# Optimization experiments

Hardware: AMD Instinct MI355X
Metric: run time of the kernel (lower is better)

The kernel has to match this reference:

```python
import jax, jax.numpy as jnp
import numpy as np

N_NODES = 100000
N_EDGES = 3200000
IN_FEATS = 512
HIDDEN = 256
N_CLASSES = 64
NITER = 10
HALT_BIAS_INIT = 3.0


def setup_inputs() -> dict:
    key = jax.random.key(0)
    ks = jax.random.split(key, 8)
    x = jax.random.normal(ks[0], (N_NODES, IN_FEATS), dtype=jnp.float32)
    edge_index = jax.random.randint(ks[1], (2, N_EDGES), 0, N_NODES, dtype=jnp.int64)
    # Linear layers: layers[0]: in->hidden, layers[1]: hidden->classes, halt: classes->1
    W0 = jax.random.normal(ks[2], (IN_FEATS, HIDDEN), dtype=jnp.float32) / np.sqrt(IN_FEATS)
    b0 = jnp.zeros((HIDDEN,), dtype=jnp.float32)
    W1 = jax.random.normal(ks[3], (HIDDEN, N_CLASSES), dtype=jnp.float32) / np.sqrt(HIDDEN)
    b1 = jnp.zeros((N_CLASSES,), dtype=jnp.float32)
    Wh = jax.random.normal(ks[4], (N_CLASSES, 1), dtype=jnp.float32) / np.sqrt(N_CLASSES)
    bh = jnp.full((1,), HALT_BIAS_INIT, dtype=jnp.float32)
    return {"x": x, "edge_index": edge_index, "edge_dropout": 0,
            "W0": W0, "b0": b0, "W1": W1, "b1": b1, "Wh": Wh, "bh": bh}


def reference(x, edge_index, edge_dropout, W0, b0, W1, b1, Wh, bh):
    N = x.shape[0]
    # MLP encoder (eval mode: dropout is identity)
    h = jax.nn.relu(x @ W0 + b0)
    h = h @ W1 + b1                                   # [N, C]

    # gcn_norm with self-loops (edge_dropout=0 in eval => identical every iter)
    loops = jnp.arange(N, dtype=edge_index.dtype)
    row = jnp.concatenate([edge_index[0], loops])     # source
    col = jnp.concatenate([edge_index[1], loops])     # target (aggregation index)
    deg = jax.ops.segment_sum(jnp.ones_like(col, dtype=h.dtype), col, num_segments=N)
    dinv = jnp.where(deg > 0, deg ** -0.5, 0.0)
    norm = dinv[row] * dinv[col]                      # [E+N]

    def step(ph, _):
        msg = norm[:, None] * ph[row]                 # gather + scale, [E+N, C]
        ph2 = jax.ops.segment_sum(msg, col, num_segments=N)  # scatter_add
        logit = jnp.clip(ph2 @ Wh + bh, -10.0, 10.0)  # [N, 1]
        return ph2, (ph2, logit)

    _, (props, logits) = jax.lax.scan(step, h, None, length=NITER)
    outputs = jnp.concatenate([h[None], props], axis=0)       # [niter+1, N, C]
    halting_logits = jnp.transpose(logits[:, :, 0])           # [N, niter]

    lam = jax.nn.sigmoid(halting_logits)
    remain = jnp.cumprod(1.0 - lam, axis=1)                   # inclusive
    remain_excl = jnp.concatenate([jnp.ones((N, 1), lam.dtype), remain[:, :-1]], axis=1)
    p = lam * remain_excl
    p = p.at[:, -1].add(remain[:, -1])                        # leftover mass to last step
    return outputs, p, halting_logits
```

## Files before the change

### kernel.cpp

```cpp
#include <hip/hip_runtime.h>
#include <hip/hip_bf16.h>

#define N_NODES  100000
#define N_EDGES  3200000
#define IN_FEATS 512
#define HIDDEN   256
#define N_CLASSES 64
#define NITER    10

#define SCAN_NB  49

#define OUT_P_OFF  ((size_t)(NITER + 1) * N_NODES * N_CLASSES)
#define OUT_HL_OFF (OUT_P_OFF + (size_t)N_NODES * NITER)

#define WS_META_INTS (4 * N_NODES + 128)
#define WS_CSR_OFF   ((size_t)WS_META_INTS * 4)
#define WS_W0F_OFF   (WS_CSR_OFF + (size_t)2 * N_EDGES * 4)
#define WS_W1F_OFF   (WS_W0F_OFF + 262144)
#define WS_SH0_OFF   (WS_W1F_OFF + 32768)
#define WS_SH1_OFF   (WS_SH0_OFF + (size_t)N_NODES * 64 * 2)
#define WS_NEED_W    (WS_SH0_OFF)
#define WS_NEED_BF   (WS_SH1_OFF + (size_t)N_NODES * 64 * 2)

typedef _Float16 f16x8 __attribute__((ext_vector_type(8)));
typedef _Float16 f16x4 __attribute__((ext_vector_type(4)));
typedef float    f32x4 __attribute__((ext_vector_type(4)));

__device__ __forceinline__ float bflo(unsigned v) { return __uint_as_float(v << 16); }
__device__ __forceinline__ float bfhi(unsigned v) { return __uint_as_float(v & 0xffff0000u); }
__device__ __forceinline__ unsigned short f2bf(float f) {
    unsigned u = __float_as_uint(f);
    return (unsigned short)((u + 0x7fffu + ((u >> 16) & 1u)) >> 16);
}

__global__ void k_detect(const int* ei, int* flag) {
    if (threadIdx.x == 0 && blockIdx.x == 0) {
        int is64 = 1;
        for (int k = 0; k < 128; ++k) {
            if (ei[2 * k + 1] != 0) { is64 = 0; break; }
        }
        *flag = is64;
    }
}

__device__ __forceinline__ int edge_row(const void* ei, int is64, int e) {
    return is64 ? (int)((const long long*)ei)[e] : ((const int*)ei)[e];
}
__device__ __forceinline__ int edge_col(const void* ei, int is64, int e) {
    return is64 ? (int)((const long long*)ei)[(size_t)N_EDGES + e]
                : ((const int*)ei)[(size_t)N_EDGES + e];
}
__device__ __forceinline__ int edge_row_nt(const void* ei, int is64, int e) {
    return is64 ? (int)__builtin_nontemporal_load((const long long*)ei + e)
                : __builtin_nontemporal_load((const int*)ei + e);
}
__device__ __forceinline__ int edge_col_nt(const void* ei, int is64, int e) {
    return is64 ? (int)__builtin_nontemporal_load((const long long*)ei + (size_t)N_EDGES + e)
                : __builtin_nontemporal_load((const int*)ei + (size_t)N_EDGES + e);
}

__global__ void k_count(const void* ei, const int* flag, int* cnt) {
    int e = blockIdx.x * 256 + threadIdx.x;
    if (e >= N_EDGES) return;
    int is64 = *flag;
    atomicAdd(&cnt[edge_col_nt(ei, is64, e)], 1);
}

__global__ __launch_bounds__(256) void k_scan1(const int* cnt, int* part) {
    __shared__ int sd[256];
    int b = blockIdx.x, t = threadIdx.x;
    int s = 0;
    for (int j = t; j < 2048; j += 256) {
        int idx = b * 2048 + j;
        if (idx < N_NODES) s += cnt[idx];
    }
    sd[t] = s;
    __syncthreads();
    for (int o = 128; o > 0; o >>= 1) {
        if (t < o) sd[t] += sd[t + o];
        __syncthreads();
    }
    if (t == 0) part[b] = sd[0];
}

__global__ __launch_bounds__(256) void k_scan2(int* part, int* offs) {
    __shared__ int sd[256];
    int t = threadIdx.x;
    sd[t] = (t < SCAN_NB) ? part[t] : 0;
    __syncthreads();
    for (int o = 1; o < 256; o <<= 1) {
        int add = (t >= o) ? sd[t - o] : 0;
        __syncthreads();
        sd[t] += add;
        __syncthreads();
    }
    if (t < SCAN_NB) part[t] = (t == 0) ? 0 : sd[t - 1];
    if (t == 0) offs[N_NODES] = N_EDGES;
}

__global__ __launch_bounds__(256) void k_scan3(const int* cnt, const int* part, int* offs) {
    __shared__ int sd[256];
    int b = blockIdx.x, t = threadIdx.x;
    int base = b * 2048 + t * 8;
    int local[8];
    int s = 0;
#pragma unroll
    for (int j = 0; j < 8; ++j) {
        int idx = base + j;
        int v = (idx < N_NODES) ? cnt[idx] : 0;
        local[j] = s;
        s += v;
    }
    sd[t] = s;
    __syncthreads();
    for (int o = 1; o < 256; o <<= 1) {
        int add = (t >= o) ? sd[t - o] : 0;
        __syncthreads();
        sd[t] += add;
        __syncthreads();
    }
    int tbase = part[b] + ((t == 0) ? 0 : sd[t - 1]);
#pragma unroll
    for (int j = 0; j < 8; ++j) {
        int idx = base + j;
        if (idx < N_NODES) offs[idx] = tbase + local[j];
    }
}

__global__ void k_dinv(const int* cnt, float* dinv) {
    int i = blockIdx.x * 256 + threadIdx.x;
    if (i >= N_NODES) return;
    dinv[i] = rsqrtf((float)(cnt[i] + 1));
}

#define FILL_GRID 3200
__global__ __launch_bounds__(256) void k_fill_part(const void* ei, const int* flag,
        const int* offs, int* cursor, int* csr) {
    const int g = blockIdx.x & 7;
    const int bi = blockIdx.x >> 3;
    const int lo = g * (N_NODES / 8);
    const int hi = lo + (N_NODES / 8);
    const int is64 = *flag;
    const int stride = (FILL_GRID >> 3) * 256;
    for (int e = bi * 256 + threadIdx.x; e < N_EDGES; e += stride) {
        int c = edge_col_nt(ei, is64, e);
        if (c >= lo && c < hi) {
            int r = edge_row_nt(ei, is64, e);
            int pos = offs[c] + atomicAdd(&cursor[c], 1);
            csr[pos] = r << 7;
        }
    }
}

__global__ void k_prep_w(const float* __restrict__ W0, const float* __restrict__ W1,
                         _Float16* __restrict__ W0f, _Float16* __restrict__ W1f) {
    int id = blockIdx.x * 256 + threadIdx.x;
    if (id < 16384) {
        int l = id & 63, c = (id >> 6) & 15, kkg = id >> 10;
        int n = c * 16 + (l & 15);
        int kb = kkg * 32 + ((l >> 4) * 8);
        f16x8 v;
#pragma unroll
        for (int j = 0; j < 8; ++j) v[j] = (_Float16)W0[(size_t)(kb + j) * HIDDEN + n];
        *(f16x8*)&W0f[(size_t)id * 8] = v;
    } else if (id < 16384 + 2048) {
        int id2 = id - 16384;
        int l = id2 & 63, c = (id2 >> 6) & 3, kkg = id2 >> 8;
        int n = c * 16 + (l & 15);
        int kb = kkg * 32 + ((l >> 4) * 8);
        f16x8 v;
#pragma unroll
        for (int j = 0; j < 8; ++j) v[j] = (_Float16)W1[(size_t)(kb + j) * N_CLASSES + n];
        *(f16x8*)&W1f[(size_t)id2 * 8] = v;
    }
}

#define EBM 64
#define XS_STRIDE 72
#define H1_STRIDE 264
#define XS0   0
#define XS1   9216
#define WST0  18432
#define WST1  34816
#define W2ST0 34816
#define W2ST1 38912
__global__ __launch_bounds__(256) void k_encoder_mfma(
        const float* __restrict__ x, const _Float16* __restrict__ W0f,
        const float* __restrict__ b0, const _Float16* __restrict__ W1f,
        const float* __restrict__ b1, float* __restrict__ out,
        const float* __restrict__ dinv,
        unsigned short* __restrict__ shadow, int write_shadow) {
    __shared__ char smem[51200];
    const int t = threadIdx.x;
    const int w = t >> 6, l = t & 63;
    const int g = l >> 4, r15 = l & 15;
    const int row0 = blockIdx.x * EBM;
    const int c4 = t & 15;
    const int srow0 = t >> 4;

    f32x4 acc[16];
#pragma unroll
    for (int c = 0; c < 16; ++c) acc[c] = (f32x4){0.f, 0.f, 0.f, 0.f};

    float4 xld[4];
    f16x8 wld[4];
#pragma unroll
    for (int q = 0; q < 4; ++q) {
        int grow = row0 + q * 16 + srow0;
        if (grow >= N_NODES) grow = N_NODES - 1;
        xld[q] = *(const float4*)&x[(size_t)grow * IN_FEATS + c4 * 4];
    }
#pragma unroll
    for (int q = 0; q < 4; ++q) wld[q] = *(const f16x8*)&W0f[(size_t)(q * 256 + t) * 8];
#pragma unroll
    for (int q = 0; q < 4; ++q) {
        f16x4 hv = {(_Float16)xld[q].x, (_Float16)xld[q].y, (_Float16)xld[q].z, (_Float16)xld[q].w};
        *(f16x4*)(smem + XS0 + ((q * 16 + srow0) * XS_STRIDE + c4 * 4) * 2) = hv;
    }
#pragma unroll
    for (int q = 0; q < 4; ++q)
        *(f16x8*)(smem + WST0 + (q * 256 + t) * 16) = wld[q];
    __syncthreads();

    for (int kkg = 0; kkg < 16; ++kkg) {
        const int kc = kkg >> 1, kk = kkg & 1;
        if (kkg < 15) {
#pragma unroll
            for (int q = 0; q < 4; ++q)
                wld[q] = *(const f16x8*)&W0f[(size_t)((kkg + 1) * 1024 + q * 256 + t) * 8];
        }
        if (kk == 0 && kc < 7) {
#pragma unroll
            for (int q = 0; q < 4; ++q) {
                int grow = row0 + q * 16 + srow0;
                if (grow >= N_NODES) grow = N_NODES - 1;
                xld[q] = *(const float4*)&x[(size_t)grow * IN_FEATS + (kc + 1) * 64 + c4 * 4];
            }
        }
        const char* xbase = smem + ((kc & 1) ? XS1 : XS0);
        const char* wbase = smem + ((kkg & 1) ? WST1 : WST0);
        f16x8 af = *(const f16x8*)(xbase + ((w * 16 + r15) * XS_STRIDE + kk * 32 + g * 8) * 2);
#pragma unroll
        for (int c = 0; c < 16; ++c) {
            f16x8 bf = *(const f16x8*)(wbase + ((c << 6) | l) * 16);
            acc[c] = __builtin_amdgcn_mfma_f32_16x16x32_f16(af, bf, acc[c], 0, 0, 0);
        }
        if (kkg < 15) {
            char* wdst = smem + ((kkg & 1) ? WST0 : WST1);
#pragma unroll
            for (int q = 0; q < 4; ++q)
                *(f16x8*)(wdst + (q * 256 + t) * 16) = wld[q];
        }
        if (kk == 1 && kc < 7) {
            char* xdst = smem + ((kc & 1) ? XS0 : XS1);
#pragma unroll
            for (int q = 0; q < 4; ++q) {
                f16x4 hv = {(_Float16)xld[q].x, (_Float16)xld[q].y, (_Float16)xld[q].z, (_Float16)xld[q].w};
                *(f16x4*)(xdst + ((q * 16 + srow0) * XS_STRIDE + c4 * 4) * 2) = hv;
            }
        }
        __syncthreads();
    }

    f16x8 w2ld = *(const f16x8*)&W1f[(size_t)t * 8];
#pragma unroll
    for (int c = 0; c < 16; ++c) {
        float bb = b0[c * 16 + r15];
#pragma unroll
        for (int i = 0; i < 4; ++i) {
            int row = w * 16 + g * 4 + i;
            *(_Float16*)(smem + (row * H1_STRIDE + c * 16 + r15) * 2) =
                (_Float16)fmaxf(acc[c][i] + bb, 0.f);
        }
    }
    *(f16x8*)(smem + W2ST0 + t * 16) = w2ld;
    __syncthreads();

    f32x4 acc2[4];
#pragma unroll
    for (int c = 0; c < 4; ++c) acc2[c] = (f32x4){0.f, 0.f, 0.f, 0.f};
    for (int kkg = 0; kkg < 8; ++kkg) {
        if (kkg < 7) w2ld = *(const f16x8*)&W1f[(size_t)((kkg + 1) * 256 + t) * 8];
        const char* wbase = smem + ((kkg & 1) ? W2ST1 : W2ST0);
        f16x8 af = *(const f16x8*)(smem + ((w * 16 + r15) * H1_STRIDE + kkg * 32 + g * 8) * 2);
#pragma unroll
        for (int c = 0; c < 4; ++c) {
            f16x8 bf = *(const f16x8*)(wbase + ((c << 6) | l) * 16);
            acc2[c] = __builtin_amdgcn_mfma_f32_16x16x32_f16(af, bf, acc2[c], 0, 0, 0);
        }
        if (kkg < 7)
            *(f16x8*)(smem + ((kkg & 1) ? W2ST0 : W2ST1) + t * 16) = w2ld;
        __syncthreads();
    }
#pragma unroll
    for (int c = 0; c < 4; ++c) {
        float bb = b1[c * 16 + r15];
#pragma unroll
        for (int i = 0; i < 4; ++i) {
            int row = row0 + w * 16 + g * 4 + i;
            if (row < N_NODES) {
                float v = acc2[c][i] + bb;
                int col = c * 16 + r15;
                out[(size_t)row * 64 + col] = v;
                if (write_shadow)
                    shadow[(size_t)row * 64 + col] = f2bf(dinv[row] * v);
            }
        }
    }
}

__global__ __launch_bounds__(256) void k_encoder(const float* __restrict__ x,
        const float* __restrict__ W0, const float* __restrict__ b0,
        const float* __restrict__ W1, const float* __restrict__ b1,
        float* __restrict__ out) {
    __shared__ float xsh[32][128];
    __shared__ float h1s[32][HIDDEN + 1];
    const int t = threadIdx.x;
    const int rg = t >> 6;
    const int cg = t & 63;
    const size_t row0 = (size_t)blockIdx.x * 32;
    float acc[8][4];
#pragma unroll
    for (int i = 0; i < 8; ++i)
        acc[i][0] = acc[i][1] = acc[i][2] = acc[i][3] = 0.f;
    for (int kc = 0; kc < 4; ++kc) {
        __syncthreads();
#pragma unroll
        for (int q = 0; q < 4; ++q) {
            int idx = t + q * 256;
            int r = idx >> 5, pos = idx & 31;
            *(float4*)&xsh[r][pos * 4] =
                *(const float4*)&x[(row0 + r) * IN_FEATS + kc * 128 + pos * 4];
        }
        __syncthreads();
        for (int kk = 0; kk < 128; kk += 4) {
            float4 xv[8];
#pragma unroll
            for (int i = 0; i < 8; ++i) xv[i] = *(const float4*)&xsh[rg * 8 + i][kk];
#pragma unroll
            for (int j = 0; j < 4; ++j) {
                float4 wv = *(const float4*)&W0[(size_t)(kc * 128 + kk + j) * HIDDEN + cg * 4];
#pragma unroll
                for (int i = 0; i < 8; ++i) {
                    float xj = (&xv[i].x)[j];
                    acc[i][0] = fmaf(xj, wv.x, acc[i][0]);
                    acc[i][1] = fmaf(xj, wv.y, acc[i][1]);
                    acc[i][2] = fmaf(xj, wv.z, acc[i][2]);
                    acc[i][3] = fmaf(xj, wv.w, acc[i][3]);
                }
            }
        }
    }
    float4 bb = *(const float4*)&b0[cg * 4];
#pragma unroll
    for (int i = 0; i < 8; ++i) {
        int r = rg * 8 + i;
        h1s[r][cg * 4 + 0] = fmaxf(acc[i][0] + bb.x, 0.f);
        h1s[r][cg * 4 + 1] = fmaxf(acc[i][1] + bb.y, 0.f);
        h1s[r][cg * 4 + 2] = fmaxf(acc[i][2] + bb.z, 0.f);
        h1s[r][cg * 4 + 3] = fmaxf(acc[i][3] + bb.w, 0.f);
    }
    __syncthreads();
    float a2[8];
#pragma unroll
    for (int i = 0; i < 8; ++i) a2[i] = 0.f;
    for (int k = 0; k < HIDDEN; ++k) {
        float wv = W1[(size_t)k * N_CLASSES + cg];
#pragma unroll
        for (int i = 0; i < 8; ++i) a2[i] = fmaf(h1s[rg * 8 + i][k], wv, a2[i]);
    }
    float bv = b1[cg];
#pragma unroll
    for (int i = 0; i < 8; ++i)
        out[(row0 + rg * 8 + i) * N_CLASSES + cg] = a2[i] + bv;
}

__global__ __launch_bounds__(256) void k_prop_s(
        const unsigned short* __restrict__ pin_s, float* __restrict__ pout,
        unsigned short* __restrict__ pout_s, const int* __restrict__ offs,
        const int* __restrict__ csr, const float* __restrict__ dinv,
        const float* __restrict__ Wh, const float* __restrict__ bh,
        float* __restrict__ hl, int t) {
    int node = (blockIdx.x * 256 + threadIdx.x) >> 5;
    if (node >= N_NODES) return;
    int hlane = threadIdx.x & 31;
    int base = threadIdx.x & 32;
    const char* gbase = (const char*)pin_s + hlane * 4;
    unsigned own = *(const unsigned*)(gbase + ((size_t)node << 7));
    float a0 = bflo(own), a1 = bfhi(own);
    float c0 = 0.f, c1 = 0.f;
    int e0 = offs[node], e1 = offs[node + 1];
    for (int eb = e0; eb < e1; eb += 32) {
        int n = e1 - eb; if (n > 32) n = 32;
        int idx = eb + hlane;
        int ew = csr[idx < e1 ? idx : e1 - 1];
        int j = 0;
        for (; j + 16 <= n; j += 16) {
            unsigned v[16];
#pragma unroll
            for (int q = 0; q < 16; ++q) {
                int s = __shfl(ew, base + j + q, 64);
                v[q] = *(const unsigned*)(gbase + s);
            }
#pragma unroll
            for (int q = 0; q < 16; ++q) {
                if (q & 1) { c0 += bflo(v[q]); c1 += bfhi(v[q]); }
                else       { a0 += bflo(v[q]); a1 += bfhi(v[q]); }
            }
        }
        for (; j + 8 <= n; j += 8) {
            unsigned v[8];
#pragma unroll
            for (int q = 0; q < 8; ++q) {
                int s = __shfl(ew, base + j + q, 64);
                v[q] = *(const unsigned*)(gbase + s);
            }
#pragma unroll
            for (int q = 0; q < 8; ++q) {
                if (q & 1) { c0 += bflo(v[q]); c1 += bfhi(v[q]); }
                else       { a0 += bflo(v[q]); a1 += bfhi(v[q]); }
            }
        }
        for (; j < n; ++j) {
            int s = __shfl(ew, base + j, 64);
            unsigned v = *(const unsigned*)(gbase + s);
            a0 += bflo(v);
            a1 += bfhi(v);
        }
    }
    float di = dinv[node];
    float fa = di * (a0 + c0), fb = di * (a1 + c1);
    *(float2*)&pout[(size_t)node * 64 + hlane * 2] = make_float2(fa, fb);
    *(unsigned*)&pout_s[(size_t)node * 64 + hlane * 2] =
        (unsigned)f2bf(di * fa) | ((unsigned)f2bf(di * fb) << 16);
    float2 wh = *(const float2*)&Wh[hlane * 2];
    float s = fa * wh.x + fb * wh.y;
#pragma unroll
    for (int o = 16; o > 0; o >>= 1) s += __shfl_xor(s, o, 64);
    if (hlane == 0) {
        float lg = s + bh[0];
        lg = fminf(10.0f, fmaxf(-10.0f, lg));
        hl[(size_t)node * NITER + t] = lg;
    }
}

__global__ __launch_bounds__(256) void k_prop(const float* __restrict__ pin,
        float* __restrict__ pout, const int* __restrict__ offs,
        const int* __restrict__ csr, const float* __restrict__ dinv,
        const float* __restrict__ Wh, const float* __restrict__ bh,
        float* __restrict__ hl, int t) {
    int wid = (blockIdx.x * blockDim.x + threadIdx.x) >> 6;
    int lane = threadIdx.x & 63;
    if (wid >= N_NODES) return;
    float di = dinv[wid];
    float a[4];
    a[0] = di * di * pin[(size_t)wid * 64 + lane];
    a[1] = a[2] = a[3] = 0.f;
    int e0 = offs[wid], e1 = offs[wid + 1];
    for (int eb = e0; eb < e1; eb += 64) {
        int n = e1 - eb; if (n > 64) n = 64;
        int idx = eb + lane;
        int ew = csr[idx < e1 ? idx : e1 - 1];
        int j = 0;
        for (; j + 8 <= n; j += 8) {
            float v[8], w[8];
#pragma unroll
            for (int q = 0; q < 8; ++q) {
                int r = __shfl(ew, j + q, 64) >> 7;
                w[q] = dinv[r] * di;
                v[q] = pin[(size_t)r * 64 + lane];
            }
#pragma unroll
            for (int q = 0; q < 8; ++q) a[q & 3] = fmaf(w[q], v[q], a[q & 3]);
        }
        for (; j < n; ++j) {
            int r = __shfl(ew, j, 64) >> 7;
            a[0] = fmaf(dinv[r] * di, pin[(size_t)r * 64 + lane], a[0]);
        }
    }
    float acc = (a[0] + a[1]) + (a[2] + a[3]);
    pout[(size_t)wid * 64 + lane] = acc;
    float s = acc * Wh[lane];
#pragma unroll
    for (int o = 32; o > 0; o >>= 1) s += __shfl_xor(s, o, 64);
    if (lane == 0) {
        float lg = s + bh[0];
        lg = fminf(10.0f, fmaxf(-10.0f, lg));
        hl[(size_t)wid * NITER + t] = lg;
    }
}

__global__ void k_p(const float* __restrict__ hl, float* __restrict__ p) {
    int i = blockIdx.x * 256 + threadIdx.x;
    if (i >= N_NODES) return;
    float remain = 1.0f;
    float pv[NITER];
#pragma unroll
    for (int t = 0; t < NITER; ++t) {
        float lg = hl[(size_t)i * NITER + t];
        float lam = 1.0f / (1.0f + expf(-lg));
        pv[t] = lam * remain;
        remain *= (1.0f - lam);
    }
    pv[NITER - 1] += remain;
#pragma unroll
    for (int t = 0; t < NITER; ++t) p[(size_t)i * NITER + t] = pv[t];
}

extern "C" void kernel_launch(void* const* d_in, const int* in_sizes, int n_in,
                              void* d_out, int out_size, void* d_ws, size_t ws_size,
                              hipStream_t stream) {
    const float* x  = (const float*)d_in[0];
    const void*  ei = d_in[1];
    const float* W0 = (const float*)d_in[3];
    const float* b0 = (const float*)d_in[4];
    const float* W1 = (const float*)d_in[5];
    const float* b1 = (const float*)d_in[6];
    const float* Wh = (const float*)d_in[7];
    const float* bh = (const float*)d_in[8];
    float* out = (float*)d_out;

    int* ws_i   = (int*)d_ws;
    int* cnt    = ws_i;
    int* offs   = ws_i + N_NODES;
    int* cursor = ws_i + 2 * N_NODES + 2;
    int* part   = ws_i + 3 * N_NODES + 2;
    int* flag   = ws_i + 3 * N_NODES + 66;
    float* dinv = (float*)(ws_i + 3 * N_NODES + 128);
    int* csr    = (int*)((char*)d_ws + WS_CSR_OFF);
    _Float16* W0f = (_Float16*)((char*)d_ws + WS_W0F_OFF);
    _Float16* W1f = (_Float16*)((char*)d_ws + WS_W1F_OFF);
    unsigned short* sh0 = (unsigned short*)((char*)d_ws + WS_SH0_OFF);
    unsigned short* sh1 = (unsigned short*)((char*)d_ws + WS_SH1_OFF);

    const int use_w  = ws_size >= WS_NEED_W;
    const int use_bf = ws_size >= WS_NEED_BF;

    hipMemsetAsync(d_ws, 0, (size_t)(3 * N_NODES + 128) * 4, stream);
    k_detect<<<1, 64, 0, stream>>>((const int*)ei, flag);
    k_count<<<(N_EDGES + 255) / 256, 256, 0, stream>>>(ei, flag, cnt);
    k_scan1<<<SCAN_NB, 256, 0, stream>>>(cnt, part);
    k_scan2<<<1, 256, 0, stream>>>(part, offs);
    k_scan3<<<SCAN_NB, 256, 0, stream>>>(cnt, part, offs);
    k_dinv<<<(N_NODES + 255) / 256, 256, 0, stream>>>(cnt, dinv);
    k_fill_part<<<FILL_GRID, 256, 0, stream>>>(ei, flag, offs, cursor, csr);

    if (use_w) {
        k_prep_w<<<72, 256, 0, stream>>>(W0, W1, W0f, W1f);
        k_encoder_mfma<<<(N_NODES + EBM - 1) / EBM, 256, 0, stream>>>(
            x, W0f, b0, W1f, b1, out, dinv, sh0, use_bf);
    } else {
        k_encoder<<<N_NODES / 32, 256, 0, stream>>>(x, W0, b0, W1, b1, out);
    }

    float* hl = out + OUT_HL_OFF;
    if (use_bf) {
        for (int it = 0; it < NITER; ++it) {
            const unsigned short* pin_s = (it & 1) ? sh1 : sh0;
            unsigned short* pout_s      = (it & 1) ? sh0 : sh1;
            float* pout = out + (size_t)(it + 1) * N_NODES * N_CLASSES;
            k_prop_s<<<((size_t)N_NODES * 32 + 255) / 256, 256, 0, stream>>>(
                pin_s, pout, pout_s, offs, csr, dinv, Wh, bh, hl, it);
        }
    } else {
        for (int it = 0; it < NITER; ++it) {
            const float* pin = out + (size_t)it * N_NODES * N_CLASSES;
            float* pout      = out + (size_t)(it + 1) * N_NODES * N_CLASSES;
            k_prop<<<((size_t)N_NODES * 64 + 255) / 256, 256, 0, stream>>>(
                pin, pout, offs, csr, dinv, Wh, bh, hl, it);
        }
    }
    k_p<<<(N_NODES + 255) / 256, 256, 0, stream>>>(hl, out + OUT_P_OFF);
}
```

Measured before the change: 1.002 ms.

## Split bf16 shadow features into 16-column quarter planes and move halting into final pass

The bf16 shadow buffer is stored as four planes of 16 columns each. The propagation kernel is reworked so that each block handles one quarter-plane for 8 nodes, with 4 edge groups gathering 32-byte rows in parallel, and blocks are interleaved so that plane-mates run together. The aim is a smaller gather working set per plane for better L2 hit rates. Halting logit computation is removed from each propagation step and folded, together with the p computation, into a single final kernel that rereads all outputs. Outputs are written with nontemporal stores. The cost is an extra full read of the propagated outputs and more blocks with cross-lane reductions.

```diff
diff --git a/kernel.cpp b/kernel.cpp
--- a/kernel.cpp
+++ b/kernel.cpp
@@ -25,6 +25,7 @@
 typedef _Float16 f16x8 __attribute__((ext_vector_type(8)));
 typedef _Float16 f16x4 __attribute__((ext_vector_type(4)));
 typedef float    f32x4 __attribute__((ext_vector_type(4)));
+typedef float    f32x2 __attribute__((ext_vector_type(2)));
 
 __device__ __forceinline__ float bflo(unsigned v) { return __uint_as_float(v << 16); }
 __device__ __forceinline__ float bfhi(unsigned v) { return __uint_as_float(v & 0xffff0000u); }
@@ -147,7 +148,7 @@
         if (c >= lo && c < hi) {
             int r = edge_row_nt(ei, is64, e);
             int pos = offs[c] + atomicAdd(&cursor[c], 1);
-            csr[pos] = r << 7;
+            csr[pos] = r << 5;
         }
     }
 }
@@ -303,7 +304,7 @@
                 int col = c * 16 + r15;
                 out[(size_t)row * 64 + col] = v;
                 if (write_shadow)
-                    shadow[(size_t)row * 64 + col] = f2bf(dinv[row] * v);
+                    shadow[((size_t)c * N_NODES + row) * 16 + r15] = f2bf(dinv[row] * v);
             }
         }
     }
@@ -375,80 +376,75 @@
         out[(row0 + rg * 8 + i) * N_CLASSES + cg] = a2[i] + bv;
 }
 
-__global__ __launch_bounds__(256) void k_prop_s(
+__global__ __launch_bounds__(256) void k_prop_q(
         const unsigned short* __restrict__ pin_s, float* __restrict__ pout,
         unsigned short* __restrict__ pout_s, const int* __restrict__ offs,
-        const int* __restrict__ csr, const float* __restrict__ dinv,
-        const float* __restrict__ Wh, const float* __restrict__ bh,
-        float* __restrict__ hl, int t) {
-    int node = (blockIdx.x * 256 + threadIdx.x) >> 5;
+        const int* __restrict__ csr, const float* __restrict__ dinv) {
+    const int b = blockIdx.x;
+    const int p = (b & 7) >> 1;
+    const int o = ((b >> 3) << 1) + (b & 1);
+    const int slot = threadIdx.x >> 5;
+    const int node = o * 8 + slot;
     if (node >= N_NODES) return;
-    int hlane = threadIdx.x & 31;
-    int base = threadIdx.x & 32;
-    const char* gbase = (const char*)pin_s + hlane * 4;
-    unsigned own = *(const unsigned*)(gbase + ((size_t)node << 7));
-    float a0 = bflo(own), a1 = bfhi(own);
-    float c0 = 0.f, c1 = 0.f;
+    const int hl32 = threadIdx.x & 31;
+    const int g2 = hl32 >> 3;
+    const int fl = hl32 & 7;
+    const int wbase = threadIdx.x & 32;
+
+    const char* qlane = (const char*)pin_s + (size_t)p * N_NODES * 32 + fl * 4;
+    float a0 = 0.f, a1 = 0.f, c0 = 0.f, c1 = 0.f;
     int e0 = offs[node], e1 = offs[node + 1];
     for (int eb = e0; eb < e1; eb += 32) {
-        int n = e1 - eb; if (n > 32) n = 32;
-        int idx = eb + hlane;
-        int ew = csr[idx < e1 ? idx : e1 - 1];
-        int j = 0;
-        for (; j + 16 <= n; j += 16) {
-            unsigned v[16];
-#pragma unroll
-            for (int q = 0; q < 16; ++q) {
-                int s = __shfl(ew, base + j + q, 64);
-                v[q] = *(const unsigned*)(gbase + s);
-            }
-#pragma unroll
-            for (int q = 0; q < 16; ++q) {
-                if (q & 1) { c0 += bflo(v[q]); c1 += bfhi(v[q]); }
-                else       { a0 += bflo(v[q]); a1 += bfhi(v[q]); }
-            }
-        }
-        for (; j + 8 <= n; j += 8) {
+        int n = e1 - eb;
+        if (n >= 32) {
+            int soff = __builtin_nontemporal_load(csr + eb + hl32);
             unsigned v[8];
 #pragma unroll
-            for (int q = 0; q < 8; ++q) {
-                int s = __shfl(ew, base + j + q, 64);
-                v[q] = *(const unsigned*)(gbase + s);
-            }
-#pragma unroll
-            for (int q = 0; q < 8; ++q) {
-                if (q & 1) { c0 += bflo(v[q]); c1 += bfhi(v[q]); }
-                else       { a0 += bflo(v[q]); a1 += bfhi(v[q]); }
-            }
-        }
-        for (; j < n; ++j) {
-            int s = __shfl(ew, base + j, 64);
-            unsigned v = *(const unsigned*)(gbase + s);
-            a0 += bflo(v);
-            a1 += bfhi(v);
-        }
-    }
-    float di = dinv[node];
-    float fa = di * (a0 + c0), fb = di * (a1 + c1);
-    *(float2*)&pout[(size_t)node * 64 + hlane * 2] = make_float2(fa, fb);
-    *(unsigned*)&pout_s[(size_t)node * 64 + hlane * 2] =
-        (unsigned)f2bf(di * fa) | ((unsigned)f2bf(di * fb) << 16);
-    float2 wh = *(const float2*)&Wh[hlane * 2];
-    float s = fa * wh.x + fb * wh.y;
-#pragma unroll
-    for (int o = 16; o > 0; o >>= 1) s += __shfl_xor(s, o, 64);
-    if (hlane == 0) {
-        float lg = s + bh[0];
-        lg = fminf(10.0f, fmaxf(-10.0f, lg));
-        hl[(size_t)node * NITER + t] = lg;
+            for (int u = 0; u < 8; ++u) {
+                int so = __shfl(soff, wbase + u * 4 + g2, 64);
+                v[u] = *(const unsigned*)(qlane + so);
+            }
+#pragma unroll
+            for (int u = 0; u < 8; ++u) {
+                if (u & 1) { c0 += bflo(v[u]); c1 += bfhi(v[u]); }
+                else       { a0 += bflo(v[u]); a1 += bfhi(v[u]); }
+            }
+        } else {
+            int idx = eb + hl32;
+            int soff = __builtin_nontemporal_load(csr + (idx < e1 ? idx : e1 - 1));
+#pragma unroll
+            for (int k = 0; k < 8; ++k) {
+                int j = g2 + 4 * k;
+                int so = __shfl(soff, wbase + j, 64);
+                if (j < n) {
+                    unsigned v = *(const unsigned*)(qlane + so);
+                    a0 += bflo(v);
+                    a1 += bfhi(v);
+                }
+            }
+        }
+    }
+    float s0 = a0 + c0, s1 = a1 + c1;
+    s0 += __shfl_xor(s0, 8, 64);  s1 += __shfl_xor(s1, 8, 64);
+    s0 += __shfl_xor(s0, 16, 64); s1 += __shfl_xor(s1, 16, 64);
+    if (hl32 < 8) {
+        unsigned own = *(const unsigned*)(qlane + ((size_t)node << 5));
+        s0 += bflo(own);
+        s1 += bfhi(own);
+        float di = dinv[node];
+        float fa = di * s0, fb = di * s1;
+        f32x2 fv = {fa, fb};
+        __builtin_nontemporal_store(fv,
+            (f32x2*)&pout[(size_t)node * 64 + p * 16 + fl * 2]);
+        unsigned pk = (unsigned)f2bf(di * fa) | ((unsigned)f2bf(di * fb) << 16);
+        __builtin_nontemporal_store(pk,
+            (unsigned*)((char*)pout_s + (size_t)p * N_NODES * 32 + ((size_t)node << 5) + fl * 4));
     }
 }
 
 __global__ __launch_bounds__(256) void k_prop(const float* __restrict__ pin,
         float* __restrict__ pout, const int* __restrict__ offs,
-        const int* __restrict__ csr, const float* __restrict__ dinv,
-        const float* __restrict__ Wh, const float* __restrict__ bh,
-        float* __restrict__ hl, int t) {
+        const int* __restrict__ csr, const float* __restrict__ dinv) {
     int wid = (blockIdx.x * blockDim.x + threadIdx.x) >> 6;
     int lane = threadIdx.x & 63;
     if (wid >= N_NODES) return;
@@ -466,7 +462,7 @@
             float v[8], w[8];
 #pragma unroll
             for (int q = 0; q < 8; ++q) {
-                int r = __shfl(ew, j + q, 64) >> 7;
+                int r = __shfl(ew, j + q, 64) >> 5;
                 w[q] = dinv[r] * di;
                 v[q] = pin[(size_t)r * 64 + lane];
             }
@@ -474,37 +470,43 @@
             for (int q = 0; q < 8; ++q) a[q & 3] = fmaf(w[q], v[q], a[q & 3]);
         }
         for (; j < n; ++j) {
-            int r = __shfl(ew, j, 64) >> 7;
+            int r = __shfl(ew, j, 64) >> 5;
             a[0] = fmaf(dinv[r] * di, pin[(size_t)r * 64 + lane], a[0]);
         }
     }
     float acc = (a[0] + a[1]) + (a[2] + a[3]);
     pout[(size_t)wid * 64 + lane] = acc;
-    float s = acc * Wh[lane];
-#pragma unroll
-    for (int o = 32; o > 0; o >>= 1) s += __shfl_xor(s, o, 64);
+}
+
+__global__ __launch_bounds__(256) void k_pfin(const float* __restrict__ outb,
+        const float* __restrict__ Wh, const float* __restrict__ bh,
+        float* __restrict__ p, float* __restrict__ hl) {
+    int node = (blockIdx.x * 256 + threadIdx.x) >> 6;
+    if (node >= N_NODES) return;
+    int lane = threadIdx.x & 63;
+    float wv = Wh[lane];
+    float bb = bh[0];
+    float remain = 1.f;
+    float pv[NITER], lg[NITER];
+#pragma unroll
+    for (int t = 0; t < NITER; ++t) {
+        float s = outb[((size_t)(t + 1) * N_NODES + node) * 64 + lane] * wv;
+#pragma unroll
+        for (int o = 32; o > 0; o >>= 1) s += __shfl_xor(s, o, 64);
+        float l = fminf(10.f, fmaxf(-10.f, s + bb));
+        lg[t] = l;
+        float lam = 1.f / (1.f + expf(-l));
+        pv[t] = lam * remain;
+        remain *= (1.f - lam);
+    }
+    pv[NITER - 1] += remain;
     if (lane == 0) {
-        float lg = s + bh[0];
-        lg = fminf(10.0f, fmaxf(-10.0f, lg));
-        hl[(size_t)wid * NITER + t] = lg;
-    }
-}
-
-__global__ void k_p(const float* __restrict__ hl, float* __restrict__ p) {
-    int i = blockIdx.x * 256 + threadIdx.x;
-    if (i >= N_NODES) return;
-    float remain = 1.0f;
-    float pv[NITER];
-#pragma unroll
-    for (int t = 0; t < NITER; ++t) {
-        float lg = hl[(size_t)i * NITER + t];
-        float lam = 1.0f / (1.0f + expf(-lg));
-        pv[t] = lam * remain;
-        remain *= (1.0f - lam);
-    }
-    pv[NITER - 1] += remain;
-#pragma unroll
-    for (int t = 0; t < NITER; ++t) p[(size_t)i * NITER + t] = pv[t];
+#pragma unroll
+        for (int t = 0; t < NITER; ++t) {
+            p[(size_t)node * NITER + t] = pv[t];
+            hl[(size_t)node * NITER + t] = lg[t];
+        }
+    }
 }
 
 extern "C" void kernel_launch(void* const* d_in, const int* in_sizes, int n_in,
@@ -553,22 +555,21 @@
         k_encoder<<<N_NODES / 32, 256, 0, stream>>>(x, W0, b0, W1, b1, out);
     }
 
-    float* hl = out + OUT_HL_OFF;
     if (use_bf) {
         for (int it = 0; it < NITER; ++it) {
             const unsigned short* pin_s = (it & 1) ? sh1 : sh0;
             unsigned short* pout_s      = (it & 1) ? sh0 : sh1;
             float* pout = out + (size_t)(it + 1) * N_NODES * N_CLASSES;
-            k_prop_s<<<((size_t)N_NODES * 32 + 255) / 256, 256, 0, stream>>>(
-                pin_s, pout, pout_s, offs, csr, dinv, Wh, bh, hl, it);
+            k_prop_q<<<50000, 256, 0, stream>>>(pin_s, pout, pout_s, offs, csr, dinv);
         }
     } else {
         for (int it = 0; it < NITER; ++it) {
             const float* pin = out + (size_t)it * N_NODES * N_CLASSES;
             float* pout      = out + (size_t)(it + 1) * N_NODES * N_CLASSES;
             k_prop<<<((size_t)N_NODES * 64 + 255) / 256, 256, 0, stream>>>(
-                pin, pout, offs, csr, dinv, Wh, bh, hl, it);
-        }
-    }
-    k_p<<<(N_NODES + 255) / 256, 256, 0, stream>>>(hl, out + OUT_P_OFF);
-}
+                pin, pout, offs, csr, dinv);
+        }
+    }
+    k_pfin<<<(N_NODES * 64 + 255) / 256, 256, 0, stream>>>(
+        out, Wh, bh, out + OUT_P_OFF, out + OUT_HL_OFF);
+}
```

New measurement: 2.000 ms. +99.7%, slower.
